# Optimization experiments

Hardware: AMD Instinct MI355X
Metric: run time of the kernel (lower is better)

## Reference

```python
import jax, jax.numpy as jnp
import numpy as np

B = 128      # number of swarms
NA = 64      # agents per swarm (na)
D = 8        # input feature dim
RD = 128     # attention hidden dim r
H = 16       # output channels h (l = sqrt(h) = 4)


def setup_inputs() -> dict:
    key = jax.random.key(0)
    ks = jax.random.split(key, 16)
    x = jax.random.normal(ks[0], (B * NA, D, NA), dtype=jnp.float32)
    L = jax.random.randint(ks[1], (B * NA, D, NA), 0, 2).astype(jnp.float32)
    p = lambda k, shp: jax.random.normal(k, shp, dtype=jnp.float32)
    return {
        "x": x, "L": L,
        "Aq": p(ks[2], (RD, D)), "Ak": p(ks[3], (RD, D)), "Av": p(ks[4], (RD, D)),
        "Aq1": p(ks[5], (RD, RD)), "Ak1": p(ks[6], (RD, RD)), "Av1": p(ks[7], (RD, RD)),
        "Aq5": p(ks[8], (RD, RD)), "Ak5": p(ks[9], (RD, RD)), "Av5": p(ks[10], (RD, RD)),
        "Ao": p(ks[11], (RD, RD)), "Ao1": p(ks[12], (RD, RD)), "Ao5": p(ks[13], (H, RD)),
    }


def _attn(Xin, Aq, Ak, Av, sqrt_nn):
    # Xin: (b, f, n); Aq/Ak/Av: (r, f); sqrt_nn: (b, 1, 1)
    Q = jax.nn.sigmoid(jnp.einsum('rf,bfn->bnr', Aq, Xin))   # Q already transposed
    K = jax.nn.sigmoid(jnp.einsum('rf,bfn->brn', Ak, Xin))
    V = jax.nn.sigmoid(jnp.einsum('rf,bfn->bnr', Av, Xin))
    S = jnp.einsum('bnr,brm->bnm', Q, K) / sqrt_nn           # (b, n, n)
    A = jax.nn.softmax(S, axis=2)
    return jnp.einsum('bnm,bmr->brn', A, V)                  # o^T: (b, r, n)


def _kron_eye2(A):
    # torch.kron(A, eye(2)) per batch: (B, n, n) -> (B, 2n, 2n)
    Bq, n, _ = A.shape
    I2 = jnp.eye(2, dtype=A.dtype)
    return (A[:, :, None, :, None] * I2[None, :, None, :]).reshape(Bq, 2 * n, 2 * n)


def reference(x, L, Aq, Ak, Av, Aq1, Ak1, Av1, Aq5, Ak5, Av5, Ao, Ao1, Ao5):
    na = x.shape[2]
    Bsw = x.shape[0] // na
    num_nb = jnp.sum((L[:, 0, :] >= 1.0).astype(jnp.float32), axis=1) + 1.0
    sqrt_nn = jnp.sqrt(num_nb)[:, None, None]                # (Bx, 1, 1)

    o = _attn(x, Aq, Ak, Av, sqrt_nn)
    R = jax.nn.silu(jnp.einsum('sr,brn->bsn', Ao, o))
    o = _attn(R, Aq1, Ak1, Av1, sqrt_nn)
    R = jax.nn.silu(jnp.einsum('sr,brn->bsn', Ao1, o))
    o = _attn(R, Aq5, Ak5, Av5, sqrt_nn)
    R = jax.nn.silu(jnp.einsum('hr,brn->bhn', Ao5, o))       # (Bx, 16, na)

    blk = lambda a, b: R[:, a:b, :].sum(axis=1).reshape(Bsw, na, na)
    R11 = _kron_eye2(blk(0, 4))
    R12 = _kron_eye2(blk(4, 8))
    R21 = _kron_eye2(blk(8, 12))
    R22 = _kron_eye2(blk(12, 16))
    # block matrix [[R11, R12], [R21, R22]] -> (Bsw, 4na, 4na)
    Rfull = jnp.concatenate(
        (jnp.concatenate((R11, R21), axis=1), jnp.concatenate((R12, R22), axis=1)),
        axis=2)

    Rfull = Rfull ** 2
    Rupper = Rfull + jnp.swapaxes(Rfull, 1, 2)
    n_tot = 4 * na
    Dg = jnp.eye(n_tot, dtype=Rupper.dtype)
    Rdiag = Rupper * (1.0 - Dg)                              # diag zeroed
    Rout = Dg * Rupper                                       # keep diag only
    rowsum = jnp.sum(Rdiag, axis=2)[:, :, None]              # (Bsw, n, 1)
    return Rout + Dg * rowsum - Rdiag
```

## Files before the change

### kernel.cpp

```cpp
#include <hip/hip_runtime.h>

typedef _Float16 f16;
typedef __attribute__((ext_vector_type(8))) _Float16 h8v;
typedef __attribute__((ext_vector_type(4))) float f4v;
typedef __attribute__((ext_vector_type(16))) float f16acc;

#define OFF_WQ  0
#define OFF_WK  2048
#define OFF_WV  4096
#define OFF_AQ1 6144
#define OFF_AK1 22528
#define OFF_AV1 38912
#define OFF_AQ5 55296
#define OFF_AK5 71680
#define OFF_AV5 88064
#define OFF_AO  104448
#define OFF_AO1 120832
#define OFF_AO5 137216
#define WTS_TOTAL 139264

#define P2 136
#define P1 72

__device__ __forceinline__ f4v mfma16_(h8v a, h8v b, f4v c) {
  return __builtin_amdgcn_mfma_f32_16x16x32_f16(a, b, c, 0, 0, 0);
}
__device__ __forceinline__ f16acc mfma32_(h8v a, h8v b, f16acc c) {
  return __builtin_amdgcn_mfma_f32_32x32x16_f16(a, b, c, 0, 0, 0);
}
__device__ __forceinline__ float rcp_(float x) { return __builtin_amdgcn_rcpf(x); }
__device__ __forceinline__ unsigned int pk2(float a, float b) {
  __fp16 __attribute__((ext_vector_type(2))) h2 = __builtin_amdgcn_cvt_pkrtz(a, b);
  return *reinterpret_cast<unsigned int*>(&h2);
}
__device__ __forceinline__ f16acc zero16() {
  f16acc z;
  #pragma unroll
  for (int i = 0; i < 16; ++i) z[i] = 0.f;
  return z;
}

template<int ACT>
__device__ __forceinline__ unsigned long long pack4act(float a, float b, float c, float d) {
  float v[4] = {a, b, c, d};
  #pragma unroll
  for (int j = 0; j < 4; ++j) {
    float t = v[j];
    if (ACT == 0)      t = rcp_(1.0f + __expf(-t));
    else if (ACT == 1) t = t * rcp_(1.0f + __expf(-t));
    v[j] = t;
  }
  union { unsigned long long u64; unsigned int u32[2]; } u;
  u.u32[0] = pk2(v[0], v[1]);
  u.u32[1] = pk2(v[2], v[3]);
  return u.u64;
}

template<int NKK>
__device__ __forceinline__ void qkv_ph(const f16* __restrict__ Wq,
                                       const f16* __restrict__ Wk,
                                       const f16* __restrict__ Wv,
                                       const f16* __restrict__ Xt,
                                       f16* __restrict__ Qt, f16* __restrict__ Kt,
                                       f16* __restrict__ Vb, int w, int lane)
{
  const int l31 = lane & 31, lh = lane >> 5;
  const int rt = w >> 1, ct = w & 1;
  const int xbase = (ct * 32 + l31) * P2 + lh * 8;
  h8v xf[NKK];
  #pragma unroll
  for (int kk = 0; kk < NKK; ++kk)
    xf[kk] = *(const h8v*)(Xt + xbase + kk * 16);
  f16acc aq = zero16(), ak = zero16(), av = zero16();
  #pragma unroll
  for (int kk = 0; kk < NKK; ++kk) {
    const int fo = (rt * NKK + kk) * 512 + lane * 8;
    h8v fq = *(const h8v*)(Wq + fo);
    h8v fk = *(const h8v*)(Wk + fo);
    h8v fv = *(const h8v*)(Wv + fo);
    aq = mfma32_(fq, xf[kk], aq);
    ak = mfma32_(fk, xf[kk], ak);
    av = mfma32_(xf[kk], fv, av);
  }
  const int nrow = (ct * 32 + l31) * P2;
  const int vrow = (rt * 32 + l31) * P1 + ct * 32 + lh * 4;
  #pragma unroll
  for (int q = 0; q < 4; ++q) {
    const int rr = rt * 32 + q * 8 + lh * 4;
    *(unsigned long long*)(Qt + nrow + rr) =
        pack4act<0>(aq[4*q], aq[4*q+1], aq[4*q+2], aq[4*q+3]);
    *(unsigned long long*)(Kt + nrow + rr) =
        pack4act<0>(ak[4*q], ak[4*q+1], ak[4*q+2], ak[4*q+3]);
    *(unsigned long long*)(Vb + vrow + q * 8) =
        pack4act<0>(av[4*q], av[4*q+1], av[4*q+2], av[4*q+3]);
  }
}

__device__ __forceinline__ void softmax_ph(const f16* __restrict__ Qt,
                                           const f16* __restrict__ Kt,
                                           f16* __restrict__ Ps,
                                           float* __restrict__ smax,
                                           float* __restrict__ ssum,
                                           float is, int w, int lane)
{
  const int lrow = lane & 15, lk = lane >> 4;
  const int nst = w & 3, mh = w >> 2;
  const int n = nst * 16 + lrow;
  h8v bq[4];
  #pragma unroll
  for (int kk = 0; kk < 4; ++kk)
    bq[kk] = *(const h8v*)(Qt + n * P2 + kk * 32 + lk * 8);
  f4v acc[2];
  #pragma unroll
  for (int t = 0; t < 2; ++t) {
    const int mt = mh * 2 + t;
    acc[t] = (f4v){0.f, 0.f, 0.f, 0.f};
    #pragma unroll
    for (int kk = 0; kk < 4; ++kk) {
      h8v a = *(const h8v*)(Kt + (mt * 16 + lrow) * P2 + kk * 32 + lk * 8);
      acc[t] = mfma16_(a, bq[kk], acc[t]);
    }
  }
  float mx = -1e30f;
  #pragma unroll
  for (int t = 0; t < 2; ++t)
    #pragma unroll
    for (int j = 0; j < 4; ++j) { acc[t][j] *= is; mx = fmaxf(mx, acc[t][j]); }
  mx = fmaxf(mx, __shfl_xor(mx, 16));
  mx = fmaxf(mx, __shfl_xor(mx, 32));
  if (lk == 0) smax[mh * 64 + n] = mx;
  __syncthreads();
  const float gmax = fmaxf(smax[n], smax[64 + n]);
  float sm = 0.f;
  #pragma unroll
  for (int t = 0; t < 2; ++t)
    #pragma unroll
    for (int j = 0; j < 4; ++j) { acc[t][j] = __expf(acc[t][j] - gmax); sm += acc[t][j]; }
  sm += __shfl_xor(sm, 16);
  sm += __shfl_xor(sm, 32);
  if (lk == 0) ssum[mh * 64 + n] = sm;
  __syncthreads();
  const float inv = rcp_(ssum[n] + ssum[64 + n]);
  #pragma unroll
  for (int t = 0; t < 2; ++t) {
    const int mt = mh * 2 + t;
    union { unsigned long long u64; unsigned int u32[2]; } u;
    u.u32[0] = pk2(acc[t][0] * inv, acc[t][1] * inv);
    u.u32[1] = pk2(acc[t][2] * inv, acc[t][3] * inv);
    *(unsigned long long*)(Ps + n * P1 + mt * 16 + lk * 4) = u.u64;
  }
}

__device__ __forceinline__ void pv_ph(const f16* __restrict__ Vb,
                                      const f16* __restrict__ Ps,
                                      f16* __restrict__ Ot, int w, int lane)
{
  const int l31 = lane & 31, lh = lane >> 5;
  const int rt = w >> 1, ct = w & 1;
  f16acc acc = zero16();
  #pragma unroll
  for (int kk = 0; kk < 4; ++kk) {
    h8v a = *(const h8v*)(Vb + (rt * 32 + l31) * P1 + kk * 16 + lh * 8);
    h8v b = *(const h8v*)(Ps + (ct * 32 + l31) * P1 + kk * 16 + lh * 8);
    acc = mfma32_(a, b, acc);
  }
  const int nrow = (ct * 32 + l31) * P2;
  #pragma unroll
  for (int q = 0; q < 4; ++q)
    *(unsigned long long*)(Ot + nrow + rt * 32 + q * 8 + lh * 4) =
        pack4act<2>(acc[4*q], acc[4*q+1], acc[4*q+2], acc[4*q+3]);
}

__device__ __forceinline__ void ao_ph(const f16* __restrict__ Ao,
                                      const f16* __restrict__ Ot,
                                      f16* __restrict__ Rt, int w, int lane)
{
  const int l31 = lane & 31, lh = lane >> 5;
  const int st = w >> 1, ct = w & 1;
  f16acc acc = zero16();
  #pragma unroll
  for (int kk = 0; kk < 8; ++kk) {
    h8v a = *(const h8v*)(Ao + (st * 8 + kk) * 512 + lane * 8);
    h8v b = *(const h8v*)(Ot + (ct * 32 + l31) * P2 + kk * 16 + lh * 8);
    acc = mfma32_(a, b, acc);
  }
  const int nrow = (ct * 32 + l31) * P2;
  #pragma unroll
  for (int q = 0; q < 4; ++q)
    *(unsigned long long*)(Rt + nrow + st * 32 + q * 8 + lh * 4) =
        pack4act<1>(acc[4*q], acc[4*q+1], acc[4*q+2], acc[4*q+3]);
}

__device__ __forceinline__ void final_ph(const f16* __restrict__ Ao5g,
                                         const f16* __restrict__ Ot,
                                         float* __restrict__ rch_b, int w, int lane)
{
  const int lrow = lane & 15, lk = lane >> 4;
  h8v a[4];
  #pragma unroll
  for (int kk = 0; kk < 4; ++kk)
    a[kk] = *(const h8v*)(Ao5g + lrow * 128 + kk * 32 + lk * 8);
  const int n = 16 * w + lrow;
  f4v acc = {0.f, 0.f, 0.f, 0.f};
  #pragma unroll
  for (int kk = 0; kk < 4; ++kk) {
    h8v b = *(const h8v*)(Ot + n * P2 + kk * 32 + lk * 8);
    acc = mfma16_(a[kk], b, acc);
  }
  #pragma unroll
  for (int j = 0; j < 4; ++j) {
    float v = acc[j];
    v = v * rcp_(1.0f + __expf(-v));
    rch_b[(lk * 4 + j) * 64 + n] = v;
  }
}

__global__ __launch_bounds__(512, 4)
void swarm_attn_mfma(const float* __restrict__ x, const float* __restrict__ L,
                     const f16* __restrict__ wts, float* __restrict__ rch)
{
  __shared__ f16 Xt[64 * P2];
  __shared__ f16 Qt[64 * P2];
  __shared__ f16 Kt[64 * P2];
  __shared__ f16 Vb[128 * P1];
  __shared__ float smax[2 * 64];
  __shared__ float ssum[2 * 64];
  __shared__ float s_inv;
  f16* Ps = Xt;

  const int b = blockIdx.x;
  const int tid = threadIdx.x;
  const int w = tid >> 6, lane = tid & 63;

  {
    const int n = tid >> 3, c = tid & 7;
    unsigned int val = 0;
    if (c < 4) {
      const float a  = x[(size_t)b * 512 + (2 * c) * 64 + n];
      const float bb = x[(size_t)b * 512 + (2 * c + 1) * 64 + n];
      val = pk2(a, bb);
    }
    *(unsigned int*)(Xt + n * P2 + 2 * c) = val;
  }
  if (w == 0) {
    const float lv = L[(size_t)b * 512 + lane];
    const unsigned long long msk = __ballot(lv >= 1.0f);
    if (lane == 0) s_inv = __frsqrt_rn((float)(__popcll(msk) + 1));
  }
  __syncthreads();
  const float is = s_inv;

  qkv_ph<1>(wts + OFF_WQ, wts + OFF_WK, wts + OFF_WV, Xt, Qt, Kt, Vb, w, lane);
  __syncthreads();
  softmax_ph(Qt, Kt, Ps, smax, ssum, is, w, lane);
  __syncthreads();
  pv_ph(Vb, Ps, Qt, w, lane);
  __syncthreads();
  ao_ph(wts + OFF_AO, Qt, Xt, w, lane);
  __syncthreads();

  qkv_ph<8>(wts + OFF_AQ1, wts + OFF_AK1, wts + OFF_AV1, Xt, Qt, Kt, Vb, w, lane);
  __syncthreads();
  softmax_ph(Qt, Kt, Ps, smax, ssum, is, w, lane);
  __syncthreads();
  pv_ph(Vb, Ps, Qt, w, lane);
  __syncthreads();
  ao_ph(wts + OFF_AO1, Qt, Xt, w, lane);
  __syncthreads();

  qkv_ph<8>(wts + OFF_AQ5, wts + OFF_AK5, wts + OFF_AV5, Xt, Qt, Kt, Vb, w, lane);
  __syncthreads();
  softmax_ph(Qt, Kt, Ps, smax, ssum, is, w, lane);
  __syncthreads();
  pv_ph(Vb, Ps, Qt, w, lane);
  __syncthreads();
  if (w < 4) final_ph(wts + OFF_AO5, Qt, rch + (size_t)b * 1024, w, lane);
}

__global__ void conv_wts(const float* Aq, const float* Ak, const float* Av,
                         const float* Aq1, const float* Ak1, const float* Av1,
                         const float* Aq5, const float* Ak5, const float* Av5,
                         const float* Ao, const float* Ao1, const float* Ao5,
                         f16* wts)
{
  const int t = blockIdx.x * 256 + threadIdx.x;
  if (t >= WTS_TOTAL) return;
  float v;
  if (t < 6144) {
    const int m = t >> 11, idx = t & 2047;
    const int fi = idx >> 9, rem = idx & 511, lane = rem >> 3, j = rem & 7;
    const int r = fi * 32 + (lane & 31), k = (lane >> 5) * 8 + j;
    const float* W = (m == 0) ? Aq : (m == 1) ? Ak : Av;
    v = (k < 8) ? W[r * 8 + k] : 0.f;
  } else if (t < 137216) {
    const int m = (t - 6144) >> 14, idx = (t - 6144) & 16383;
    const int fi = idx >> 9, rem = idx & 511, lane = rem >> 3, j = rem & 7;
    const int rt = fi >> 3, kk = fi & 7;
    const int r = rt * 32 + (lane & 31), k = kk * 16 + (lane >> 5) * 8 + j;
    const float* W = (m == 0) ? Aq1 : (m == 1) ? Ak1 : (m == 2) ? Av1 :
                     (m == 3) ? Aq5 : (m == 4) ? Ak5 : (m == 5) ? Av5 :
                     (m == 6) ? Ao : Ao1;
    v = W[r * 128 + k];
  } else {
    v = Ao5[t - 137216];
  }
  wts[t] = (f16)v;
}

#define ASTR 65
__global__ __launch_bounds__(256, 1)
void reduce_kernel(const float* __restrict__ rch, float* __restrict__ Mw,
                   float* __restrict__ rsw, float* __restrict__ csw)
{
  __shared__ float Msh[4 * 64 * ASTR];
  const int s = blockIdx.x, t = threadIdx.x;
  for (int e = t; e < 16384; e += 256) {
    const int j = e & 63, i = (e >> 6) & 63, g = e >> 12;
    const float* p = rch + ((size_t)s * 64 + i) * 1024 + (4 * g) * 64 + j;
    const float v = p[0] + p[64] + p[128] + p[192];
    Msh[(g * 64 + i) * ASTR + j] = v;
    Mw[(size_t)s * 16384 + e] = v;
  }
  __syncthreads();
  const int g = t >> 6, i = t & 63;
  float r2 = 0.f, c2 = 0.f;
  for (int j = 0; j < 64; ++j) {
    const float a = Msh[(g * 64 + i) * ASTR + j];
    const float bb = Msh[(g * 64 + j) * ASTR + i];
    r2 = fmaf(a, a, r2);
    c2 = fmaf(bb, bb, c2);
  }
  rsw[s * 256 + g * 64 + i] = r2;
  csw[s * 256 + g * 64 + i] = c2;
}

__global__ __launch_bounds__(256, 1)
void expand_kernel(const float* __restrict__ Mw, const float* __restrict__ rsw,
                   const float* __restrict__ csw, float* __restrict__ out)
{
  const size_t e = ((size_t)blockIdx.x * 256 + threadIdx.x) * 4;
  const int s = (int)(e >> 16);
  const int rem = (int)(e & 65535);
  const int u = rem >> 8, v0 = rem & 255;
  const int ub = u >> 7, ii = (u & 127) >> 1, p = u & 1;
  const float* Ms = Mw + (size_t)s * 16384;
  float4 o;
  float* po = &o.x;
  #pragma unroll
  for (int c = 0; c < 4; ++c) {
    const int v = v0 + c;
    const int vb = v >> 7, jj = (v & 127) >> 1, q = v & 1;
    float val = 0.f;
    if (u == v) {
      val = rsw[s * 256 + (2 * ub) * 64 + ii] + rsw[s * 256 + (2 * ub + 1) * 64 + ii]
          + csw[s * 256 + ub * 64 + ii] + csw[s * 256 + (2 + ub) * 64 + ii];
    } else if (p == q) {
      const int g = 2 * ub + vb, gp = 2 * vb + ub;
      const float a = Ms[g * 4096 + ii * 64 + jj];
      const float bb = Ms[gp * 4096 + jj * 64 + ii];
      val = -(a * a + bb * bb);
    }
    po[c] = val;
  }
  *(float4*)(out + e) = o;
}

extern "C" void kernel_launch(void* const* d_in, const int* in_sizes, int n_in,
                              void* d_out, int out_size, void* d_ws, size_t ws_size,
                              hipStream_t stream)
{
  const float* x   = (const float*)d_in[0];
  const float* L   = (const float*)d_in[1];
  const float* Aq  = (const float*)d_in[2];
  const float* Ak  = (const float*)d_in[3];
  const float* Av  = (const float*)d_in[4];
  const float* Aq1 = (const float*)d_in[5];
  const float* Ak1 = (const float*)d_in[6];
  const float* Av1 = (const float*)d_in[7];
  const float* Aq5 = (const float*)d_in[8];
  const float* Ak5 = (const float*)d_in[9];
  const float* Av5 = (const float*)d_in[10];
  const float* Ao  = (const float*)d_in[11];
  const float* Ao1 = (const float*)d_in[12];
  const float* Ao5 = (const float*)d_in[13];

  f16* wts = (f16*)d_ws;
  float* Mw  = (float*)((char*)d_ws + (size_t)WTS_TOTAL * 2);
  float* rsw = Mw + (size_t)128 * 16384;
  float* csw = rsw + 128 * 256;
  float* rch = (float*)d_out;

  conv_wts<<<(WTS_TOTAL + 255) / 256, 256, 0, stream>>>(Aq, Ak, Av, Aq1, Ak1, Av1,
                                                        Aq5, Ak5, Av5, Ao, Ao1, Ao5, wts);
  swarm_attn_mfma<<<8192, 512, 0, stream>>>(x, L, wts, rch);
  reduce_kernel<<<128, 256, 0, stream>>>(rch, Mw, rsw, csw);
  expand_kernel<<<8192, 256, 0, stream>>>(Mw, rsw, csw, (float*)d_out);
}
```

Baseline: 335.9 us.

## Cut LDS to two buffers, merge softmax syncs, fold exp2 scaling into weights

Shared memory drops from three 64x136 buffers to two by ping-ponging Q/K/X and P/O between them. Q is written after an extra barrier so it can overwrite its input X. Launch bounds rise from 4 to 6 blocks per CU. The softmax now keeps a per-half running max and sum and joins them with a single barrier instead of two. The -log2(e) factor is folded into the Q/K/V weights at conversion time so sigmoid uses exp2 directly, and MFMA loops get s_setprio raises. These changes aim at higher occupancy and fewer barriers, at the cost of one added sync in the QKV phase and possible register pressure under the tighter launch bounds.

```diff
diff --git a/kernel.cpp b/kernel.cpp
--- a/kernel.cpp
+++ b/kernel.cpp
@@ -29,6 +29,13 @@
   return __builtin_amdgcn_mfma_f32_32x32x16_f16(a, b, c, 0, 0, 0);
 }
 __device__ __forceinline__ float rcp_(float x) { return __builtin_amdgcn_rcpf(x); }
+__device__ __forceinline__ float ex2_(float x) {
+#if __has_builtin(__builtin_amdgcn_exp2f)
+  return __builtin_amdgcn_exp2f(x);
+#else
+  return __expf(x * 0.6931471805599453f);
+#endif
+}
 __device__ __forceinline__ unsigned int pk2(float a, float b) {
   __fp16 __attribute__((ext_vector_type(2))) h2 = __builtin_amdgcn_cvt_pkrtz(a, b);
   return *reinterpret_cast<unsigned int*>(&h2);
@@ -46,8 +53,8 @@
   #pragma unroll
   for (int j = 0; j < 4; ++j) {
     float t = v[j];
-    if (ACT == 0)      t = rcp_(1.0f + __expf(-t));
-    else if (ACT == 1) t = t * rcp_(1.0f + __expf(-t));
+    if (ACT == 0)      t = rcp_(1.0f + ex2_(t));
+    else if (ACT == 1) t = t * rcp_(1.0f + ex2_(t * -1.44269504f));
     v[j] = t;
   }
   union { unsigned long long u64; unsigned int u32[2]; } u;
@@ -60,48 +67,47 @@
 __device__ __forceinline__ void qkv_ph(const f16* __restrict__ Wq,
                                        const f16* __restrict__ Wk,
                                        const f16* __restrict__ Wv,
-                                       const f16* __restrict__ Xt,
-                                       f16* __restrict__ Qt, f16* __restrict__ Kt,
-                                       f16* __restrict__ Vb, int w, int lane)
+                                       const f16* Xt, f16* Qt,
+                                       f16* __restrict__ Kt, f16* __restrict__ Vb,
+                                       int w, int lane)
 {
   const int l31 = lane & 31, lh = lane >> 5;
   const int rt = w >> 1, ct = w & 1;
   const int xbase = (ct * 32 + l31) * P2 + lh * 8;
-  h8v xf[NKK];
-  #pragma unroll
-  for (int kk = 0; kk < NKK; ++kk)
-    xf[kk] = *(const h8v*)(Xt + xbase + kk * 16);
   f16acc aq = zero16(), ak = zero16(), av = zero16();
+  __builtin_amdgcn_s_setprio(1);
   #pragma unroll
   for (int kk = 0; kk < NKK; ++kk) {
+    h8v xf = *(const h8v*)(Xt + xbase + kk * 16);
     const int fo = (rt * NKK + kk) * 512 + lane * 8;
     h8v fq = *(const h8v*)(Wq + fo);
     h8v fk = *(const h8v*)(Wk + fo);
     h8v fv = *(const h8v*)(Wv + fo);
-    aq = mfma32_(fq, xf[kk], aq);
-    ak = mfma32_(fk, xf[kk], ak);
-    av = mfma32_(xf[kk], fv, av);
-  }
+    aq = mfma32_(fq, xf, aq);
+    ak = mfma32_(fk, xf, ak);
+    av = mfma32_(xf, fv, av);
+  }
+  __builtin_amdgcn_s_setprio(0);
   const int nrow = (ct * 32 + l31) * P2;
   const int vrow = (rt * 32 + l31) * P1 + ct * 32 + lh * 4;
   #pragma unroll
   for (int q = 0; q < 4; ++q) {
-    const int rr = rt * 32 + q * 8 + lh * 4;
-    *(unsigned long long*)(Qt + nrow + rr) =
-        pack4act<0>(aq[4*q], aq[4*q+1], aq[4*q+2], aq[4*q+3]);
-    *(unsigned long long*)(Kt + nrow + rr) =
+    *(unsigned long long*)(Kt + nrow + rt * 32 + q * 8 + lh * 4) =
         pack4act<0>(ak[4*q], ak[4*q+1], ak[4*q+2], ak[4*q+3]);
     *(unsigned long long*)(Vb + vrow + q * 8) =
         pack4act<0>(av[4*q], av[4*q+1], av[4*q+2], av[4*q+3]);
   }
+  __syncthreads();
+  #pragma unroll
+  for (int q = 0; q < 4; ++q)
+    *(unsigned long long*)(Qt + nrow + rt * 32 + q * 8 + lh * 4) =
+        pack4act<0>(aq[4*q], aq[4*q+1], aq[4*q+2], aq[4*q+3]);
 }
 
 __device__ __forceinline__ void softmax_ph(const f16* __restrict__ Qt,
                                            const f16* __restrict__ Kt,
-                                           f16* __restrict__ Ps,
-                                           float* __restrict__ smax,
-                                           float* __restrict__ ssum,
-                                           float is, int w, int lane)
+                                           f16* Ps, float2* __restrict__ mxsm,
+                                           float is2, int w, int lane)
 {
   const int lrow = lane & 15, lk = lane >> 4;
   const int nst = w & 3, mh = w >> 2;
@@ -111,6 +117,7 @@
   for (int kk = 0; kk < 4; ++kk)
     bq[kk] = *(const h8v*)(Qt + n * P2 + kk * 32 + lk * 8);
   f4v acc[2];
+  __builtin_amdgcn_s_setprio(1);
   #pragma unroll
   for (int t = 0; t < 2; ++t) {
     const int mt = mh * 2 + t;
@@ -121,32 +128,33 @@
       acc[t] = mfma16_(a, bq[kk], acc[t]);
     }
   }
+  __builtin_amdgcn_s_setprio(0);
   float mx = -1e30f;
   #pragma unroll
   for (int t = 0; t < 2; ++t)
     #pragma unroll
-    for (int j = 0; j < 4; ++j) { acc[t][j] *= is; mx = fmaxf(mx, acc[t][j]); }
+    for (int j = 0; j < 4; ++j) { acc[t][j] *= is2; mx = fmaxf(mx, acc[t][j]); }
   mx = fmaxf(mx, __shfl_xor(mx, 16));
   mx = fmaxf(mx, __shfl_xor(mx, 32));
-  if (lk == 0) smax[mh * 64 + n] = mx;
-  __syncthreads();
-  const float gmax = fmaxf(smax[n], smax[64 + n]);
   float sm = 0.f;
   #pragma unroll
   for (int t = 0; t < 2; ++t)
     #pragma unroll
-    for (int j = 0; j < 4; ++j) { acc[t][j] = __expf(acc[t][j] - gmax); sm += acc[t][j]; }
+    for (int j = 0; j < 4; ++j) { acc[t][j] = ex2_(acc[t][j] - mx); sm += acc[t][j]; }
   sm += __shfl_xor(sm, 16);
   sm += __shfl_xor(sm, 32);
-  if (lk == 0) ssum[mh * 64 + n] = sm;
-  __syncthreads();
-  const float inv = rcp_(ssum[n] + ssum[64 + n]);
+  if (lk == 0) mxsm[mh * 64 + n] = make_float2(mx, sm);
+  __syncthreads();
+  const float2 s0 = mxsm[n], s1 = mxsm[64 + n];
+  const float gmax = fmaxf(s0.x, s1.x);
+  const float tot = s0.y * ex2_(s0.x - gmax) + s1.y * ex2_(s1.x - gmax);
+  const float corr = ex2_(mx - gmax) * rcp_(tot);
   #pragma unroll
   for (int t = 0; t < 2; ++t) {
     const int mt = mh * 2 + t;
     union { unsigned long long u64; unsigned int u32[2]; } u;
-    u.u32[0] = pk2(acc[t][0] * inv, acc[t][1] * inv);
-    u.u32[1] = pk2(acc[t][2] * inv, acc[t][3] * inv);
+    u.u32[0] = pk2(acc[t][0] * corr, acc[t][1] * corr);
+    u.u32[1] = pk2(acc[t][2] * corr, acc[t][3] * corr);
     *(unsigned long long*)(Ps + n * P1 + mt * 16 + lk * 4) = u.u64;
   }
 }
@@ -158,12 +166,14 @@
   const int l31 = lane & 31, lh = lane >> 5;
   const int rt = w >> 1, ct = w & 1;
   f16acc acc = zero16();
+  __builtin_amdgcn_s_setprio(1);
   #pragma unroll
   for (int kk = 0; kk < 4; ++kk) {
     h8v a = *(const h8v*)(Vb + (rt * 32 + l31) * P1 + kk * 16 + lh * 8);
     h8v b = *(const h8v*)(Ps + (ct * 32 + l31) * P1 + kk * 16 + lh * 8);
     acc = mfma32_(a, b, acc);
   }
+  __builtin_amdgcn_s_setprio(0);
   const int nrow = (ct * 32 + l31) * P2;
   #pragma unroll
   for (int q = 0; q < 4; ++q)
@@ -178,12 +188,14 @@
   const int l31 = lane & 31, lh = lane >> 5;
   const int st = w >> 1, ct = w & 1;
   f16acc acc = zero16();
+  __builtin_amdgcn_s_setprio(1);
   #pragma unroll
   for (int kk = 0; kk < 8; ++kk) {
     h8v a = *(const h8v*)(Ao + (st * 8 + kk) * 512 + lane * 8);
     h8v b = *(const h8v*)(Ot + (ct * 32 + l31) * P2 + kk * 16 + lh * 8);
     acc = mfma32_(a, b, acc);
   }
+  __builtin_amdgcn_s_setprio(0);
   const int nrow = (ct * 32 + l31) * P2;
   #pragma unroll
   for (int q = 0; q < 4; ++q)
@@ -210,23 +222,19 @@
   #pragma unroll
   for (int j = 0; j < 4; ++j) {
     float v = acc[j];
-    v = v * rcp_(1.0f + __expf(-v));
+    v = v * rcp_(1.0f + ex2_(v * -1.44269504f));
     rch_b[(lk * 4 + j) * 64 + n] = v;
   }
 }
 
-__global__ __launch_bounds__(512, 4)
+__global__ __launch_bounds__(512, 6)
 void swarm_attn_mfma(const float* __restrict__ x, const float* __restrict__ L,
                      const f16* __restrict__ wts, float* __restrict__ rch)
 {
-  __shared__ f16 Xt[64 * P2];
-  __shared__ f16 Qt[64 * P2];
-  __shared__ f16 Kt[64 * P2];
+  __shared__ f16 Ab[64 * P2];
+  __shared__ f16 Bb[64 * P2];
   __shared__ f16 Vb[128 * P1];
-  __shared__ float smax[2 * 64];
-  __shared__ float ssum[2 * 64];
-  __shared__ float s_inv;
-  f16* Ps = Xt;
+  __shared__ float2 mxsm[128];
 
   const int b = blockIdx.x;
   const int tid = threadIdx.x;
@@ -240,41 +248,38 @@
       const float bb = x[(size_t)b * 512 + (2 * c + 1) * 64 + n];
       val = pk2(a, bb);
     }
-    *(unsigned int*)(Xt + n * P2 + 2 * c) = val;
-  }
-  if (w == 0) {
-    const float lv = L[(size_t)b * 512 + lane];
-    const unsigned long long msk = __ballot(lv >= 1.0f);
-    if (lane == 0) s_inv = __frsqrt_rn((float)(__popcll(msk) + 1));
-  }
-  __syncthreads();
-  const float is = s_inv;
-
-  qkv_ph<1>(wts + OFF_WQ, wts + OFF_WK, wts + OFF_WV, Xt, Qt, Kt, Vb, w, lane);
-  __syncthreads();
-  softmax_ph(Qt, Kt, Ps, smax, ssum, is, w, lane);
-  __syncthreads();
-  pv_ph(Vb, Ps, Qt, w, lane);
-  __syncthreads();
-  ao_ph(wts + OFF_AO, Qt, Xt, w, lane);
-  __syncthreads();
-
-  qkv_ph<8>(wts + OFF_AQ1, wts + OFF_AK1, wts + OFF_AV1, Xt, Qt, Kt, Vb, w, lane);
-  __syncthreads();
-  softmax_ph(Qt, Kt, Ps, smax, ssum, is, w, lane);
-  __syncthreads();
-  pv_ph(Vb, Ps, Qt, w, lane);
-  __syncthreads();
-  ao_ph(wts + OFF_AO1, Qt, Xt, w, lane);
-  __syncthreads();
-
-  qkv_ph<8>(wts + OFF_AQ5, wts + OFF_AK5, wts + OFF_AV5, Xt, Qt, Kt, Vb, w, lane);
-  __syncthreads();
-  softmax_ph(Qt, Kt, Ps, smax, ssum, is, w, lane);
-  __syncthreads();
-  pv_ph(Vb, Ps, Qt, w, lane);
-  __syncthreads();
-  if (w < 4) final_ph(wts + OFF_AO5, Qt, rch + (size_t)b * 1024, w, lane);
+    *(unsigned int*)(Ab + n * P2 + 2 * c) = val;
+  }
+  const float lv = L[(size_t)b * 512 + lane];
+  const unsigned long long msk = __ballot(lv >= 1.0f);
+  const float is2 = __frsqrt_rn((float)(__popcll(msk) + 1)) * 1.44269504f;
+  __syncthreads();
+
+  qkv_ph<1>(wts + OFF_WQ, wts + OFF_WK, wts + OFF_WV, Ab, Ab, Bb, Vb, w, lane);
+  __syncthreads();
+  softmax_ph(Ab, Bb, Bb, mxsm, is2, w, lane);
+  __syncthreads();
+  pv_ph(Vb, Bb, Ab, w, lane);
+  __syncthreads();
+  ao_ph(wts + OFF_AO, Ab, Bb, w, lane);
+  __syncthreads();
+
+  qkv_ph<8>(wts + OFF_AQ1, wts + OFF_AK1, wts + OFF_AV1, Bb, Bb, Ab, Vb, w, lane);
+  __syncthreads();
+  softmax_ph(Bb, Ab, Ab, mxsm, is2, w, lane);
+  __syncthreads();
+  pv_ph(Vb, Ab, Bb, w, lane);
+  __syncthreads();
+  ao_ph(wts + OFF_AO1, Bb, Ab, w, lane);
+  __syncthreads();
+
+  qkv_ph<8>(wts + OFF_AQ5, wts + OFF_AK5, wts + OFF_AV5, Ab, Ab, Bb, Vb, w, lane);
+  __syncthreads();
+  softmax_ph(Ab, Bb, Bb, mxsm, is2, w, lane);
+  __syncthreads();
+  pv_ph(Vb, Bb, Ab, w, lane);
+  __syncthreads();
+  if (w < 4) final_ph(wts + OFF_AO5, Ab, rch + (size_t)b * 1024, w, lane);
 }
 
 __global__ void conv_wts(const float* Aq, const float* Ak, const float* Av,
@@ -283,6 +288,7 @@
                          const float* Ao, const float* Ao1, const float* Ao5,
                          f16* wts)
 {
+  const float SCL = -1.44269504088896f;
   const int t = blockIdx.x * 256 + threadIdx.x;
   if (t >= WTS_TOTAL) return;
   float v;
@@ -291,7 +297,7 @@
     const int fi = idx >> 9, rem = idx & 511, lane = rem >> 3, j = rem & 7;
     const int r = fi * 32 + (lane & 31), k = (lane >> 5) * 8 + j;
     const float* W = (m == 0) ? Aq : (m == 1) ? Ak : Av;
-    v = (k < 8) ? W[r * 8 + k] : 0.f;
+    v = (k < 8) ? W[r * 8 + k] * SCL : 0.f;
   } else if (t < 137216) {
     const int m = (t - 6144) >> 14, idx = (t - 6144) & 16383;
     const int fi = idx >> 9, rem = idx & 511, lane = rem >> 3, j = rem & 7;
@@ -301,6 +307,7 @@
                      (m == 3) ? Aq5 : (m == 4) ? Ak5 : (m == 5) ? Av5 :
                      (m == 6) ? Ao : Ao1;
     v = W[r * 128 + k];
+    if (m < 6) v *= SCL;
   } else {
     v = Ao5[t - 137216];
   }
```

After: 716.5 us. +113.3%, slower.

## Fold log2e into weights, use exp2, drop softmax max pass

Applied to the files above, without the earlier changes.

The -log2(e) factor is folded into the Q/K/V weights during conversion, so sigmoid becomes 1/(1+exp2(acc)), and exp2 is used for SiLU and softmax too. The softmax no longer subtracts a row max, which removes one shared-memory round trip and one block barrier per attention stage. The scale factor is now computed by every wave, so the shared s_inv is gone, and the X fragments are loaded inside the QKV loop to lower register pressure. The trade-off is that softmax without a max shift depends on scores staying bounded; this holds because Q and K come from sigmoids, but large unnormalised sums could overflow exp2 when the neighbour count is small.

```diff
diff --git a/kernel.cpp b/kernel.cpp
--- a/kernel.cpp
+++ b/kernel.cpp
@@ -29,6 +29,13 @@
   return __builtin_amdgcn_mfma_f32_32x32x16_f16(a, b, c, 0, 0, 0);
 }
 __device__ __forceinline__ float rcp_(float x) { return __builtin_amdgcn_rcpf(x); }
+__device__ __forceinline__ float ex2_(float x) {
+#if __has_builtin(__builtin_amdgcn_exp2f)
+  return __builtin_amdgcn_exp2f(x);
+#else
+  return __expf(x * 0.6931471805599453f);
+#endif
+}
 __device__ __forceinline__ unsigned int pk2(float a, float b) {
   __fp16 __attribute__((ext_vector_type(2))) h2 = __builtin_amdgcn_cvt_pkrtz(a, b);
   return *reinterpret_cast<unsigned int*>(&h2);
@@ -46,8 +53,8 @@
   #pragma unroll
   for (int j = 0; j < 4; ++j) {
     float t = v[j];
-    if (ACT == 0)      t = rcp_(1.0f + __expf(-t));
-    else if (ACT == 1) t = t * rcp_(1.0f + __expf(-t));
+    if (ACT == 0)      t = rcp_(1.0f + ex2_(t));
+    else if (ACT == 1) t = t * rcp_(1.0f + ex2_(t * -1.44269504f));
     v[j] = t;
   }
   union { unsigned long long u64; unsigned int u32[2]; } u;
@@ -67,20 +74,17 @@
   const int l31 = lane & 31, lh = lane >> 5;
   const int rt = w >> 1, ct = w & 1;
   const int xbase = (ct * 32 + l31) * P2 + lh * 8;
-  h8v xf[NKK];
-  #pragma unroll
-  for (int kk = 0; kk < NKK; ++kk)
-    xf[kk] = *(const h8v*)(Xt + xbase + kk * 16);
   f16acc aq = zero16(), ak = zero16(), av = zero16();
   #pragma unroll
   for (int kk = 0; kk < NKK; ++kk) {
+    h8v xf = *(const h8v*)(Xt + xbase + kk * 16);
     const int fo = (rt * NKK + kk) * 512 + lane * 8;
     h8v fq = *(const h8v*)(Wq + fo);
     h8v fk = *(const h8v*)(Wk + fo);
     h8v fv = *(const h8v*)(Wv + fo);
-    aq = mfma32_(fq, xf[kk], aq);
-    ak = mfma32_(fk, xf[kk], ak);
-    av = mfma32_(xf[kk], fv, av);
+    aq = mfma32_(fq, xf, aq);
+    ak = mfma32_(fk, xf, ak);
+    av = mfma32_(xf, fv, av);
   }
   const int nrow = (ct * 32 + l31) * P2;
   const int vrow = (rt * 32 + l31) * P1 + ct * 32 + lh * 4;
@@ -98,10 +102,8 @@
 
 __device__ __forceinline__ void softmax_ph(const f16* __restrict__ Qt,
                                            const f16* __restrict__ Kt,
-                                           f16* __restrict__ Ps,
-                                           float* __restrict__ smax,
-                                           float* __restrict__ ssum,
-                                           float is, int w, int lane)
+                                           f16* Ps, float* __restrict__ ssum,
+                                           float is2, int w, int lane)
 {
   const int lrow = lane & 15, lk = lane >> 4;
   const int nst = w & 3, mh = w >> 2;
@@ -121,21 +123,11 @@
       acc[t] = mfma16_(a, bq[kk], acc[t]);
     }
   }
-  float mx = -1e30f;
+  float sm = 0.f;
   #pragma unroll
   for (int t = 0; t < 2; ++t)
     #pragma unroll
-    for (int j = 0; j < 4; ++j) { acc[t][j] *= is; mx = fmaxf(mx, acc[t][j]); }
-  mx = fmaxf(mx, __shfl_xor(mx, 16));
-  mx = fmaxf(mx, __shfl_xor(mx, 32));
-  if (lk == 0) smax[mh * 64 + n] = mx;
-  __syncthreads();
-  const float gmax = fmaxf(smax[n], smax[64 + n]);
-  float sm = 0.f;
-  #pragma unroll
-  for (int t = 0; t < 2; ++t)
-    #pragma unroll
-    for (int j = 0; j < 4; ++j) { acc[t][j] = __expf(acc[t][j] - gmax); sm += acc[t][j]; }
+    for (int j = 0; j < 4; ++j) { acc[t][j] = ex2_(acc[t][j] * is2); sm += acc[t][j]; }
   sm += __shfl_xor(sm, 16);
   sm += __shfl_xor(sm, 32);
   if (lk == 0) ssum[mh * 64 + n] = sm;
@@ -210,7 +202,7 @@
   #pragma unroll
   for (int j = 0; j < 4; ++j) {
     float v = acc[j];
-    v = v * rcp_(1.0f + __expf(-v));
+    v = v * rcp_(1.0f + ex2_(v * -1.44269504f));
     rch_b[(lk * 4 + j) * 64 + n] = v;
   }
 }
@@ -223,9 +215,7 @@
   __shared__ f16 Qt[64 * P2];
   __shared__ f16 Kt[64 * P2];
   __shared__ f16 Vb[128 * P1];
-  __shared__ float smax[2 * 64];
   __shared__ float ssum[2 * 64];
-  __shared__ float s_inv;
   f16* Ps = Xt;
 
   const int b = blockIdx.x;
@@ -242,17 +232,14 @@
     }
     *(unsigned int*)(Xt + n * P2 + 2 * c) = val;
   }
-  if (w == 0) {
-    const float lv = L[(size_t)b * 512 + lane];
-    const unsigned long long msk = __ballot(lv >= 1.0f);
-    if (lane == 0) s_inv = __frsqrt_rn((float)(__popcll(msk) + 1));
-  }
-  __syncthreads();
-  const float is = s_inv;
+  const float lv = L[(size_t)b * 512 + lane];
+  const unsigned long long msk = __ballot(lv >= 1.0f);
+  const float is2 = __frsqrt_rn((float)(__popcll(msk) + 1)) * 1.44269504f;
+  __syncthreads();
 
   qkv_ph<1>(wts + OFF_WQ, wts + OFF_WK, wts + OFF_WV, Xt, Qt, Kt, Vb, w, lane);
   __syncthreads();
-  softmax_ph(Qt, Kt, Ps, smax, ssum, is, w, lane);
+  softmax_ph(Qt, Kt, Ps, ssum, is2, w, lane);
   __syncthreads();
   pv_ph(Vb, Ps, Qt, w, lane);
   __syncthreads();
@@ -261,7 +248,7 @@
 
   qkv_ph<8>(wts + OFF_AQ1, wts + OFF_AK1, wts + OFF_AV1, Xt, Qt, Kt, Vb, w, lane);
   __syncthreads();
-  softmax_ph(Qt, Kt, Ps, smax, ssum, is, w, lane);
+  softmax_ph(Qt, Kt, Ps, ssum, is2, w, lane);
   __syncthreads();
   pv_ph(Vb, Ps, Qt, w, lane);
   __syncthreads();
@@ -270,7 +257,7 @@
 
   qkv_ph<8>(wts + OFF_AQ5, wts + OFF_AK5, wts + OFF_AV5, Xt, Qt, Kt, Vb, w, lane);
   __syncthreads();
-  softmax_ph(Qt, Kt, Ps, smax, ssum, is, w, lane);
+  softmax_ph(Qt, Kt, Ps, ssum, is2, w, lane);
   __syncthreads();
   pv_ph(Vb, Ps, Qt, w, lane);
   __syncthreads();
@@ -283,6 +270,7 @@
                          const float* Ao, const float* Ao1, const float* Ao5,
                          f16* wts)
 {
+  const float SCL = -1.44269504088896f;
   const int t = blockIdx.x * 256 + threadIdx.x;
   if (t >= WTS_TOTAL) return;
   float v;
@@ -291,7 +279,7 @@
     const int fi = idx >> 9, rem = idx & 511, lane = rem >> 3, j = rem & 7;
     const int r = fi * 32 + (lane & 31), k = (lane >> 5) * 8 + j;
     const float* W = (m == 0) ? Aq : (m == 1) ? Ak : Av;
-    v = (k < 8) ? W[r * 8 + k] : 0.f;
+    v = (k < 8) ? W[r * 8 + k] * SCL : 0.f;
   } else if (t < 137216) {
     const int m = (t - 6144) >> 14, idx = (t - 6144) & 16383;
     const int fi = idx >> 9, rem = idx & 511, lane = rem >> 3, j = rem & 7;
@@ -301,6 +289,7 @@
                      (m == 3) ? Aq5 : (m == 4) ? Ak5 : (m == 5) ? Av5 :
                      (m == 6) ? Ao : Ao1;
     v = W[r * 128 + k];
+    if (m < 6) v *= SCL;
   } else {
     v = Ao5[t - 137216];
   }
```

New measurement: 320.7 us. -4.5%, faster.
